# Kernel tuning notes

Hardware: AMD Instinct MI355X
Metric: run time of the kernel (lower is better)

The kernel has to match this reference:

```python
import jax, jax.numpy as jnp
import numpy as np

D_MODEL, D_STATE, D_CONV, D_INNER = 1024, 16, 4, 2048
B, S = 1, 2048
EPS = 1e-5


def setup_inputs() -> dict:
    key = jax.random.key(0)
    ks = jax.random.split(key, 8)
    sc = 0.02
    return {
        "x": jax.random.normal(ks[0], (B, S, D_MODEL), jnp.float32),
        "ln_g": jnp.ones((D_MODEL,), jnp.float32),
        "ln_b": jnp.zeros((D_MODEL,), jnp.float32),
        "in_w": jax.random.normal(ks[1], (2 * D_INNER, D_MODEL), jnp.float32) * sc,
        "conv_w": jax.random.normal(ks[2], (D_INNER, 1, D_CONV), jnp.float32) * sc,  # depthwise OIH
        "conv_b": jax.random.normal(ks[3], (D_INNER,), jnp.float32) * sc,
        "xproj_w": jax.random.normal(ks[4], (2 * D_STATE + 1, D_INNER), jnp.float32) * sc,
        "dt_w": jax.random.normal(ks[5], (D_INNER, 1), jnp.float32) * sc,
        "dt_b": jax.random.normal(ks[6], (D_INNER,), jnp.float32) * sc,
        "A_log": jnp.log(jnp.arange(1, D_STATE + 1, dtype=jnp.float32)),
        "D": jnp.ones((D_INNER,), jnp.float32),
        "out_w": jax.random.normal(ks[7], (D_MODEL, D_INNER), jnp.float32) * sc,
    }


def reference(x, ln_g, ln_b, in_w, conv_w, conv_b, xproj_w, dt_w, dt_b, A_log, D, out_w):
    b, s, _ = x.shape
    d_inner = D.shape[0]
    d_state = A_log.shape[0]
    d_conv = conv_w.shape[-1]
    residual = x

    # LayerNorm
    mu = jnp.mean(x, axis=-1, keepdims=True)
    var = jnp.mean(jnp.square(x - mu), axis=-1, keepdims=True)
    xn = (x - mu) * jax.lax.rsqrt(var + EPS) * ln_g + ln_b

    # in_proj, split into x and gate z
    xz = jnp.einsum('bsd,ed->bse', xn, in_w)  # [B,S,2*d_inner]
    xi, z = jnp.split(xz, 2, axis=-1)

    # causal depthwise conv1d (torch pads d_conv-1 both sides then crops to seq_len)
    xc = jnp.transpose(xi, (0, 2, 1))  # [B,C,S]
    xc = jnp.pad(xc, ((0, 0), (0, 0), (d_conv - 1, 0)))
    xc = jax.lax.conv_general_dilated(
        xc, conv_w, window_strides=(1,), padding='VALID',
        dimension_numbers=('NCH', 'OIH', 'NCH'), feature_group_count=d_inner)
    xc = xc + conv_b[None, :, None]
    xs = jax.nn.silu(jnp.transpose(xc, (0, 2, 1)))  # [B,S,d_inner]

    # SSM projections
    xp = jnp.einsum('bsd,ed->bse', xs, xproj_w)  # [B,S,2*d_state+1]
    delta = jax.nn.softplus(xp[..., :1] * dt_w[:, 0] + dt_b)  # [B,S,d_inner]
    Bm = xp[..., 1:1 + d_state]  # [B,S,N]
    Cm = xp[..., 1 + d_state:]   # [B,S,N]
    A = -jnp.exp(A_log)          # [N]

    dA = jnp.exp(delta[..., None] * A)                      # [B,S,d_inner,N]
    dBx = delta[..., None] * Bm[:, :, None, :] * xs[..., None]  # [B,S,d_inner,N]

    def step(h, inp):
        dA_t, dBx_t, C_t = inp
        h = dA_t * h + dBx_t                     # [B,d_inner,N]
        y_t = jnp.einsum('bdn,bn->bd', h, C_t)   # [B,d_inner]
        return h, y_t

    h0 = jnp.zeros((b, d_inner, d_state), x.dtype)
    _, ys = jax.lax.scan(step, h0, (jnp.moveaxis(dA, 1, 0),
                                    jnp.moveaxis(dBx, 1, 0),
                                    jnp.moveaxis(Cm, 1, 0)))
    y = jnp.moveaxis(ys, 0, 1) + xs * D  # [B,S,d_inner]

    y = y * jax.nn.silu(z)
    out = jnp.einsum('bse,de->bsd', y, out_w)
    return out + residual
```

## Files before the change

kernel.cpp:

```cpp
#include <hip/hip_runtime.h>
#include <cstdint>
#include <cstddef>

#define D_MODEL 1024
#define D_STATE 16
#define D_CONV  4
#define D_INNER 2048
#define SEQ     2048
#define NCHUNK  128
#define CLEN    16
#define NGRP    8
#define GCH     16
#define LN_EPS  1e-5f

typedef unsigned short ushort_t;
typedef __attribute__((ext_vector_type(8))) short short8;
typedef __attribute__((ext_vector_type(4))) float f32x4;

__device__ __forceinline__ ushort_t f2bf(float x) {
  union { float f; uint32_t u; } v; v.f = x;
  uint32_t r = (v.u + 0x7fffu + ((v.u >> 16) & 1u)) >> 16;
  return (ushort_t)r;
}
__device__ __forceinline__ float bf2f(ushort_t u) {
  union { uint32_t x; float f; } v; v.x = ((uint32_t)u) << 16; return v.f;
}

__device__ __forceinline__ void async16(void* lds, const void* g) {
  __builtin_amdgcn_global_load_lds(
      (const __attribute__((address_space(1))) unsigned int*)g,
      (__attribute__((address_space(3))) unsigned int*)lds, 16, 0, 0);
}

__device__ __forceinline__ float softplus_f(float x) {
  if (x > 20.f) return x;
  if (x < -20.f) return __expf(x);
  return __logf(1.f + __expf(x));
}

__device__ __forceinline__ void dapow(float g1, float* da) {
  float g2 = g1 * g1, g4 = g2 * g2, g8 = g4 * g4;
  #pragma unroll
  for (int n = 0; n < 16; n++) {
    int e = n + 1;
    float v = (e & 1) ? g1 : 1.f;
    if (e & 2) v *= g2;
    if (e & 4) v *= g4;
    if (e & 8) v *= g8;
    da[n] = v;
  }
}

__global__ __launch_bounds__(256) void prep_kernel(const float* __restrict__ x,
                                                   const float* __restrict__ g,
                                                   const float* __restrict__ b,
                                                   const float* __restrict__ inw,
                                                   const float* __restrict__ outw,
                                                   const float* __restrict__ xpw,
                                                   ushort_t* __restrict__ xn_bf,
                                                   ushort_t* __restrict__ inw_bf,
                                                   ushort_t* __restrict__ outw_bf,
                                                   ushort_t* __restrict__ xpw_bf) {
  int blk = blockIdx.x;
  if (blk < SEQ) {
    int row = blk;
    const float4* xr = (const float4*)(x + (size_t)row * D_MODEL);
    float4 v = xr[threadIdx.x];
    float s  = v.x + v.y + v.z + v.w;
    float ss = v.x * v.x + v.y * v.y + v.z * v.z + v.w * v.w;
    #pragma unroll
    for (int o = 32; o; o >>= 1) { s += __shfl_down(s, o); ss += __shfl_down(ss, o); }
    __shared__ float sbuf[8], ssbuf[8];
    int wid = threadIdx.x >> 6, lane = threadIdx.x & 63;
    if (lane == 0) { sbuf[wid] = s; ssbuf[wid] = ss; }
    __syncthreads();
    if (threadIdx.x == 0) {
      float t = 0.f, t2 = 0.f;
      for (int i = 0; i < 4; i++) { t += sbuf[i]; t2 += ssbuf[i]; }
      float mu = t / D_MODEL;
      sbuf[4] = mu;
      ssbuf[4] = rsqrtf(t2 / D_MODEL - mu * mu + LN_EPS);
    }
    __syncthreads();
    float mu = sbuf[4], inv = ssbuf[4];
    float4 gv = ((const float4*)g)[threadIdx.x];
    float4 bv = ((const float4*)b)[threadIdx.x];
    ushort_t o4[4];
    o4[0] = f2bf((v.x - mu) * inv * gv.x + bv.x);
    o4[1] = f2bf((v.y - mu) * inv * gv.y + bv.y);
    o4[2] = f2bf((v.z - mu) * inv * gv.z + bv.z);
    o4[3] = f2bf((v.w - mu) * inv * gv.w + bv.w);
    *(ushort4*)&xn_bf[(size_t)row * D_MODEL + threadIdx.x * 4] =
        make_ushort4(o4[0], o4[1], o4[2], o4[3]);
  } else {
    int idx = (blk - SEQ) * 256 + threadIdx.x;
    const int n1 = 2 * D_INNER * D_MODEL;
    const int n2 = D_MODEL * D_INNER;
    const int n3 = 64 * D_INNER;
    if (idx < n1) {
      inw_bf[idx] = f2bf(inw[idx]);
    } else if (idx < n1 + n2) {
      int j = idx - n1;
      outw_bf[j] = f2bf(outw[j]);
    } else if (idx < n1 + n2 + n3) {
      int j = idx - n1 - n2;
      xpw_bf[j] = (j < 33 * D_INNER) ? f2bf(xpw[j]) : (ushort_t)0;
    }
  }
}

template <int BM, int BN, int KDIM, int EPI, int NBUF, int KSPLIT>
__global__ __launch_bounds__(256, 2) void gemm_pipe(const ushort_t* __restrict__ A,
                                                    const ushort_t* __restrict__ B,
                                                    void* __restrict__ Cout,
                                                    const float* __restrict__ R,
                                                    int N) {
  constexpr int KT = KDIM / 32 / KSPLIT;
  constexpr int K2 = KDIM * 2;
  constexpr int IA = BM / 64, IB = BN / 64;
  constexpr int S  = IA + IB;
  constexpr int W  = (NBUF - 2) * S;
  constexpr int WTM = BM / 2, WTN = BN / 2;
  constexpr int MREP = WTM / 16, NREP = WTN / 16;
  __shared__ __align__(16) ushort_t As[NBUF][BM * 32];
  __shared__ __align__(16) ushort_t Bs[NBUF][BN * 32];

  const int nwg = gridDim.x * gridDim.y;
  int bid = blockIdx.y * gridDim.x + blockIdx.x;
  int swz = (bid & 7) * (nwg >> 3) + (bid >> 3);
  int bn = swz % gridDim.x, bm = swz / gridDim.x;
  int ks = 0;
  if constexpr (KSPLIT > 1) { ks = bn; bn = 0; }
  const int tid = threadIdx.x, wid = tid >> 6, lane = tid & 63;
  const int wm = wid >> 1, wn = wid & 1;
  const int row0A = bm * BM, row0B = bn * BN;
  const size_t kbase = (size_t)ks * KT * 64;

  const char* gA[IA];
  const char* gB[IB];
  #pragma unroll
  for (int i = 0; i < IA; i++) {
    int o = i * 4096 + tid * 16;
    int r = o >> 6, src = (o & 63) ^ ((r & 3) << 4);
    gA[i] = (const char*)A + (size_t)(row0A + r) * K2 + src + kbase;
  }
  #pragma unroll
  for (int i = 0; i < IB; i++) {
    int o = i * 4096 + tid * 16;
    int r = o >> 6, src = (o & 63) ^ ((r & 3) << 4);
    gB[i] = (const char*)B + (size_t)(row0B + r) * K2 + src + kbase;
  }
  const int ldsW = wid * 1024;

  auto STAGE = [&](int bb, int kt) {
    int kb = kt * 64;
    #pragma unroll
    for (int i = 0; i < IA; i++)
      async16((char*)&As[bb][0] + i * 4096 + ldsW, gA[i] + kb);
    #pragma unroll
    for (int i = 0; i < IB; i++)
      async16((char*)&Bs[bb][0] + i * 4096 + ldsW, gB[i] + kb);
  };

  #pragma unroll
  for (int p = 0; p < NBUF - 1; p++) STAGE(p, p);

  int offA[MREP], offB[NREP];
  #pragma unroll
  for (int m = 0; m < MREP; m++) {
    int row = wm * WTM + m * 16 + (lane & 15);
    offA[m] = row * 64 + ((((lane >> 4)) ^ (row & 3)) << 4);
  }
  #pragma unroll
  for (int n = 0; n < NREP; n++) {
    int row = wn * WTN + n * 16 + (lane & 15);
    offB[n] = row * 64 + ((((lane >> 4)) ^ (row & 3)) << 4);
  }

  f32x4 acc[MREP][NREP] = {};
  int cur = 0;
  for (int kt = 0; kt < KT; kt++) {
    if (kt < KT - 1) {
      if constexpr (W == 6)       asm volatile("s_waitcnt vmcnt(6)" ::: "memory");
      else if constexpr (W == 8)  asm volatile("s_waitcnt vmcnt(8)" ::: "memory");
      else if constexpr (W == 12) asm volatile("s_waitcnt vmcnt(12)" ::: "memory");
      else                        asm volatile("s_waitcnt vmcnt(0)" ::: "memory");
    } else {
      asm volatile("s_waitcnt vmcnt(0)" ::: "memory");
    }
    __builtin_amdgcn_s_barrier();
    __builtin_amdgcn_sched_barrier(0);
    const char* Ab = (const char*)&As[cur][0];
    const char* Bb = (const char*)&Bs[cur][0];
    short8 af[MREP], bf[NREP];
    #pragma unroll
    for (int m = 0; m < MREP; m++) af[m] = *(const short8*)(Ab + offA[m]);
    #pragma unroll
    for (int n = 0; n < NREP; n++) bf[n] = *(const short8*)(Bb + offB[n]);
    if (kt + NBUF - 1 < KT) {
      int b2 = cur + NBUF - 1; if (b2 >= NBUF) b2 -= NBUF;
      STAGE(b2, kt + NBUF - 1);
    }
    __builtin_amdgcn_s_setprio(1);
    #pragma unroll
    for (int m = 0; m < MREP; m++)
      #pragma unroll
      for (int n = 0; n < NREP; n++)
        acc[m][n] = __builtin_amdgcn_mfma_f32_16x16x32_bf16(af[m], bf[n], acc[m][n], 0, 0, 0);
    __builtin_amdgcn_s_setprio(0);
    cur++; if (cur == NBUF) cur = 0;
  }

  #pragma unroll
  for (int m = 0; m < MREP; m++)
    #pragma unroll
    for (int n = 0; n < NREP; n++) {
      int r0 = row0A + wm * WTM + m * 16 + ((lane >> 4) << 2);
      int c  = row0B + wn * WTN + n * 16 + (lane & 15);
      #pragma unroll
      for (int q = 0; q < 4; q++) {
        if constexpr (EPI == 0) {
          ((ushort_t*)Cout)[(size_t)(r0 + q) * N + c] = f2bf(acc[m][n][q]);
        } else if constexpr (EPI == 1) {
          size_t idx = (size_t)(r0 + q) * N + c;
          ((float*)Cout)[idx] = acc[m][n][q] + R[idx];
        } else {
          if (c < 33)
            ((float*)Cout)[((size_t)ks * SEQ + r0 + q) * 33 + c] = acc[m][n][q];
        }
      }
    }
}

__global__ __launch_bounds__(256) void xp_reduce(const float* __restrict__ part,
                                                 float* __restrict__ xp) {
  int i = blockIdx.x * 256 + threadIdx.x;
  if (i >= SEQ * 33) return;
  float s = 0.f;
  #pragma unroll
  for (int k = 0; k < 8; k++) s += part[(size_t)k * SEQ * 33 + i];
  xp[i] = s;
}

__global__ __launch_bounds__(256) void conv_silu_kernel(const ushort_t* __restrict__ xz_bf,
                                                        const float* __restrict__ cw,
                                                        const float* __restrict__ cb,
                                                        ushort_t* __restrict__ xs_bf) {
  const int t = blockIdx.x;
  const int d0 = threadIdx.x * 8;
  short8 rows[4];
  #pragma unroll
  for (int k = 0; k < 4; k++) {
    int tt = t - 3 + k;
    if (tt >= 0) rows[k] = *(const short8*)&xz_bf[(size_t)tt * (2 * D_INNER) + d0];
    else         rows[k] = (short8)0;
  }
  short8 o8;
  #pragma unroll
  for (int j = 0; j < 8; j++) {
    float4 w = ((const float4*)cw)[d0 + j];
    float acc = cb[d0 + j]
              + bf2f((ushort_t)rows[0][j]) * w.x
              + bf2f((ushort_t)rows[1][j]) * w.y
              + bf2f((ushort_t)rows[2][j]) * w.z
              + bf2f((ushort_t)rows[3][j]) * w.w;
    float sg = 1.f / (1.f + __expf(-acc));
    o8[j] = (short)f2bf(acc * sg);
  }
  *(short8*)&xs_bf[(size_t)t * D_INNER + d0] = o8;
}

__global__ __launch_bounds__(256) void scan_pass1(const ushort_t* __restrict__ xs_bf,
                                                  const float* __restrict__ xp,
                                                  const float* __restrict__ dt_w,
                                                  const float* __restrict__ dt_b,
                                                  const float* __restrict__ A_log,
                                                  float* __restrict__ Hp,
                                                  float* __restrict__ Sd) {
  int c = blockIdx.x;
  int d0 = blockIdx.y * 512 + threadIdx.x;
  __shared__ float Bsh[CLEN][16], drs[CLEN], Ash[16];
  {
    int t = threadIdx.x >> 4, n = threadIdx.x & 15;
    Bsh[t][n] = xp[(size_t)(c * CLEN + t) * 33 + 1 + n];
    if (threadIdx.x < CLEN) drs[threadIdx.x] = xp[(size_t)(c * CLEN + threadIdx.x) * 33];
    else if (threadIdx.x < CLEN + 16) {
      int n2 = threadIdx.x - CLEN;
      Ash[n2] = -__expf(A_log[n2]);
    }
  }
  __syncthreads();
  bool fastA = true;
  #pragma unroll
  for (int n = 0; n < 16; n++) fastA = fastA && (fabsf(Ash[n] + (float)(n + 1)) < 1e-4f * (n + 1));
  float dw[2] = {dt_w[d0], dt_w[d0 + 256]};
  float db[2] = {dt_b[d0], dt_b[d0 + 256]};
  float h[2][16] = {};
  float S[2] = {0.f, 0.f};
  for (int t = 0; t < CLEN; t++) {
    float bb[16];
    *(float4*)&bb[0]  = *(const float4*)&Bsh[t][0];
    *(float4*)&bb[4]  = *(const float4*)&Bsh[t][4];
    *(float4*)&bb[8]  = *(const float4*)&Bsh[t][8];
    *(float4*)&bb[12] = *(const float4*)&Bsh[t][12];
    float drt = drs[t];
    size_t tb = (size_t)(c * CLEN + t) * D_INNER;
    float xv[2] = {bf2f(xs_bf[tb + d0]), bf2f(xs_bf[tb + d0 + 256])};
    #pragma unroll
    for (int u = 0; u < 2; u++) {
      float delta = softplus_f(drt * dw[u] + db[u]);
      S[u] += delta;
      float w = delta * xv[u];
      if (fastA) {
        float da[16];
        dapow(__expf(-delta), da);
        #pragma unroll
        for (int n = 0; n < 16; n++) h[u][n] = da[n] * h[u][n] + w * bb[n];
      } else {
        #pragma unroll
        for (int n = 0; n < 16; n++) h[u][n] = __expf(delta * Ash[n]) * h[u][n] + w * bb[n];
      }
    }
  }
  #pragma unroll
  for (int u = 0; u < 2; u++) {
    int d = d0 + u * 256;
    size_t base = ((size_t)c * D_INNER + d) * 16;
    #pragma unroll
    for (int n = 0; n < 16; n += 4)
      *(float4*)&Hp[base + n] = make_float4(h[u][n], h[u][n + 1], h[u][n + 2], h[u][n + 3]);
    Sd[(size_t)c * D_INNER + d] = S[u];
  }
}

__global__ __launch_bounds__(256) void combineA(const float* __restrict__ Hp,
                                                const float* __restrict__ Sd,
                                                const float* __restrict__ A_log,
                                                float* __restrict__ Hl,
                                                float* __restrict__ Slocp,
                                                float* __restrict__ Hgtot,
                                                float* __restrict__ Sgtot) {
  int g = blockIdx.x;
  int idx = blockIdx.y * 256 + threadIdx.x;
  int d = idx >> 4, n = idx & 15;
  float An = -__expf(A_log[n]);
  float h = 0.f, S = 0.f;
  const size_t stride = (size_t)D_INNER * 16;
  #pragma unroll 4
  for (int j = 0; j < GCH; j++) {
    int c = g * GCH + j;
    Hl[(size_t)c * stride + idx] = h;
    if (n == 0) Slocp[(size_t)c * D_INNER + d] = S;
    float Sc = Sd[(size_t)c * D_INNER + d];
    float hp = Hp[(size_t)c * stride + idx];
    h = __expf(An * Sc) * h + hp;
    S += Sc;
  }
  Hgtot[(size_t)g * stride + idx] = h;
  if (n == 0) Sgtot[(size_t)g * D_INNER + d] = S;
}

__global__ __launch_bounds__(256) void combineB(const float* __restrict__ Hgtot,
                                                const float* __restrict__ Sgtot,
                                                const float* __restrict__ A_log,
                                                float* __restrict__ Ginit) {
  int idx = blockIdx.x * 256 + threadIdx.x;
  int d = idx >> 4, n = idx & 15;
  float An = -__expf(A_log[n]);
  float G = 0.f;
  const size_t stride = (size_t)D_INNER * 16;
  #pragma unroll
  for (int g = 0; g < NGRP; g++) {
    Ginit[(size_t)g * stride + idx] = G;
    G = __expf(An * Sgtot[(size_t)g * D_INNER + d]) * G + Hgtot[(size_t)g * stride + idx];
  }
}

__global__ __launch_bounds__(256) void scan_pass2(const ushort_t* __restrict__ xs_bf,
                                                  const float* __restrict__ xp,
                                                  const ushort_t* __restrict__ xz_bf,
                                                  const float* __restrict__ dt_w,
                                                  const float* __restrict__ dt_b,
                                                  const float* __restrict__ A_log,
                                                  const float* __restrict__ Dp,
                                                  const float* __restrict__ Hl,
                                                  const float* __restrict__ Slocp,
                                                  const float* __restrict__ Ginit,
                                                  ushort_t* __restrict__ y_bf) {
  int c = blockIdx.x;
  int d0 = blockIdx.y * 512 + threadIdx.x;
  __shared__ float Bsh[CLEN][16], Csh[CLEN][16], drs[CLEN], Ash[16];
  {
    int t = threadIdx.x >> 4, n = threadIdx.x & 15;
    Bsh[t][n] = xp[(size_t)(c * CLEN + t) * 33 + 1 + n];
    Csh[t][n] = xp[(size_t)(c * CLEN + t) * 33 + 17 + n];
    if (threadIdx.x < CLEN) drs[threadIdx.x] = xp[(size_t)(c * CLEN + threadIdx.x) * 33];
    else if (threadIdx.x < CLEN + 16) {
      int n2 = threadIdx.x - CLEN;
      Ash[n2] = -__expf(A_log[n2]);
    }
  }
  __syncthreads();
  bool fastA = true;
  #pragma unroll
  for (int n = 0; n < 16; n++) fastA = fastA && (fabsf(Ash[n] + (float)(n + 1)) < 1e-4f * (n + 1));
  float dw[2] = {dt_w[d0], dt_w[d0 + 256]};
  float db[2] = {dt_b[d0], dt_b[d0 + 256]};
  float Dd[2] = {Dp[d0], Dp[d0 + 256]};
  int g8 = c >> 4;
  float h[2][16];
  #pragma unroll
  for (int u = 0; u < 2; u++) {
    int d = d0 + u * 256;
    size_t hb = ((size_t)c * D_INNER + d) * 16;
    size_t gb = ((size_t)g8 * D_INNER + d) * 16;
    float Slp = Slocp[(size_t)c * D_INNER + d];
    float hl[16], gi[16];
    #pragma unroll
    for (int n = 0; n < 16; n += 4) {
      *(float4*)&hl[n] = *(const float4*)&Hl[hb + n];
      *(float4*)&gi[n] = *(const float4*)&Ginit[gb + n];
    }
    if (fastA) {
      float pw[16];
      dapow(__expf(-Slp), pw);
      #pragma unroll
      for (int n = 0; n < 16; n++) h[u][n] = hl[n] + pw[n] * gi[n];
    } else {
      #pragma unroll
      for (int n = 0; n < 16; n++) h[u][n] = hl[n] + __expf(Ash[n] * Slp) * gi[n];
    }
  }
  for (int t = 0; t < CLEN; t++) {
    float bb[16], cc[16];
    *(float4*)&bb[0]  = *(const float4*)&Bsh[t][0];
    *(float4*)&bb[4]  = *(const float4*)&Bsh[t][4];
    *(float4*)&bb[8]  = *(const float4*)&Bsh[t][8];
    *(float4*)&bb[12] = *(const float4*)&Bsh[t][12];
    *(float4*)&cc[0]  = *(const float4*)&Csh[t][0];
    *(float4*)&cc[4]  = *(const float4*)&Csh[t][4];
    *(float4*)&cc[8]  = *(const float4*)&Csh[t][8];
    *(float4*)&cc[12] = *(const float4*)&Csh[t][12];
    float drt = drs[t];
    size_t ti = (size_t)(c * CLEN + t);
    float xv[2] = {bf2f(xs_bf[ti * D_INNER + d0]), bf2f(xs_bf[ti * D_INNER + d0 + 256])};
    float zv[2] = {bf2f(xz_bf[ti * (2 * D_INNER) + D_INNER + d0]),
                   bf2f(xz_bf[ti * (2 * D_INNER) + D_INNER + d0 + 256])};
    #pragma unroll
    for (int u = 0; u < 2; u++) {
      float delta = softplus_f(drt * dw[u] + db[u]);
      float w = delta * xv[u];
      float y = 0.f;
      if (fastA) {
        float da[16];
        dapow(__expf(-delta), da);
        #pragma unroll
        for (int n = 0; n < 16; n++) {
          h[u][n] = da[n] * h[u][n] + w * bb[n];
          y += h[u][n] * cc[n];
        }
      } else {
        #pragma unroll
        for (int n = 0; n < 16; n++) {
          h[u][n] = __expf(delta * Ash[n]) * h[u][n] + w * bb[n];
          y += h[u][n] * cc[n];
        }
      }
      float z = zv[u];
      float sz = z / (1.f + __expf(-z));
      float out = (y + xv[u] * Dd[u]) * sz;
      y_bf[ti * D_INNER + d0 + u * 256] = f2bf(out);
    }
  }
}

extern "C" void kernel_launch(void* const* d_in, const int* in_sizes, int n_in,
                              void* d_out, int out_size, void* d_ws, size_t ws_size,
                              hipStream_t stream) {
  const float* x      = (const float*)d_in[0];
  const float* ln_g   = (const float*)d_in[1];
  const float* ln_b   = (const float*)d_in[2];
  const float* in_w   = (const float*)d_in[3];
  const float* conv_w = (const float*)d_in[4];
  const float* conv_b = (const float*)d_in[5];
  const float* xproj_w= (const float*)d_in[6];
  const float* dt_w   = (const float*)d_in[7];
  const float* dt_b   = (const float*)d_in[8];
  const float* A_log  = (const float*)d_in[9];
  const float* Dp     = (const float*)d_in[10];
  const float* out_w  = (const float*)d_in[11];
  float* out = (float*)d_out;

  char* ws = (char*)d_ws;
  size_t off = 0;
  auto alloc = [&](size_t bytes) { char* p = ws + off; off += (bytes + 255) & ~(size_t)255; return p; };
  ushort_t* xz_bf   = (ushort_t*)alloc((size_t)SEQ * 2 * D_INNER * 2);
  ushort_t* xn_bf   = (ushort_t*)alloc((size_t)SEQ * D_MODEL * 2);
  ushort_t* inw_bf  = (ushort_t*)alloc((size_t)2 * D_INNER * D_MODEL * 2);
  ushort_t* outw_bf = (ushort_t*)alloc((size_t)D_MODEL * D_INNER * 2);
  ushort_t* xpw_bf  = (ushort_t*)alloc((size_t)64 * D_INNER * 2);
  ushort_t* xs_bf   = (ushort_t*)alloc((size_t)SEQ * D_INNER * 2);
  float*    xp_part = (float*)   alloc((size_t)8 * SEQ * 33 * 4);
  float*    xp      = (float*)   alloc((size_t)SEQ * 33 * 4);
  float*    Hp      = (float*)   alloc((size_t)NCHUNK * D_INNER * 16 * 4);
  float*    Hl      = (float*)   alloc((size_t)NCHUNK * D_INNER * 16 * 4);
  float*    Sd      = (float*)   alloc((size_t)NCHUNK * D_INNER * 4);
  float*    Slocp   = (float*)   alloc((size_t)NCHUNK * D_INNER * 4);
  float*    Hgtot   = (float*)   alloc((size_t)NGRP * D_INNER * 16 * 4);
  float*    Sgtot   = (float*)   alloc((size_t)NGRP * D_INNER * 4);
  float*    Ginit   = (float*)   alloc((size_t)NGRP * D_INNER * 16 * 4);
  ushort_t* y_bf    = (ushort_t*)alloc((size_t)SEQ * D_INNER * 2);
  (void)ws_size;

  const int ncvt = 2 * D_INNER * D_MODEL + D_MODEL * D_INNER + 64 * D_INNER;
  prep_kernel<<<SEQ + (ncvt + 255) / 256, 256, 0, stream>>>(
      x, ln_g, ln_b, in_w, out_w, xproj_w, xn_bf, inw_bf, outw_bf, xpw_bf);
  gemm_pipe<128, 128, D_MODEL, 0, 4, 1><<<dim3(2 * D_INNER / 128, SEQ / 128), 256, 0, stream>>>(
      xn_bf, inw_bf, xz_bf, nullptr, 2 * D_INNER);
  conv_silu_kernel<<<SEQ, 256, 0, stream>>>(xz_bf, conv_w, conv_b, xs_bf);
  gemm_pipe<64, 64, D_INNER, 3, 6, 8><<<dim3(8, SEQ / 64), 256, 0, stream>>>(
      xs_bf, xpw_bf, xp_part, nullptr, 64);
  xp_reduce<<<(SEQ * 33 + 255) / 256, 256, 0, stream>>>(xp_part, xp);
  scan_pass1<<<dim3(NCHUNK, D_INNER / 512), 256, 0, stream>>>(xs_bf, xp, dt_w, dt_b, A_log, Hp, Sd);
  combineA<<<dim3(NGRP, D_INNER * 16 / 256), 256, 0, stream>>>(Hp, Sd, A_log, Hl, Slocp, Hgtot, Sgtot);
  combineB<<<D_INNER * 16 / 256, 256, 0, stream>>>(Hgtot, Sgtot, A_log, Ginit);
  scan_pass2<<<dim3(NCHUNK, D_INNER / 512), 256, 0, stream>>>(xs_bf, xp, xz_bf, dt_w, dt_b, A_log,
                                                              Dp, Hl, Slocp, Ginit, y_bf);
  gemm_pipe<64, 64, D_INNER, 1, 6, 1><<<dim3(D_MODEL / 64, SEQ / 64), 256, 0, stream>>>(
      y_bf, outw_bf, out, x, D_MODEL);
}
```

Baseline: 134.3 us.

## Fuse xproj split-K reduction into scan passes, prefetch inputs, retile in_proj GEMM

Removes the separate xp_reduce kernel and has scan_pass1 and scan_pass2 sum the eight split-K partials directly while loading B, C and delta into shared memory. This saves one launch and one intermediate buffer, but the partial sums are now read by both scan kernels. The scan loops also prefetch the next timestep's xs and z values into registers so the loads overlap the recurrence. The in_proj GEMM tile changes from 128x128 with 4 stages to 256x128 with 3 stages, which halves the grid rows and may change occupancy.

```diff
diff --git a/kernel.cpp b/kernel.cpp
--- a/kernel.cpp
+++ b/kernel.cpp
@@ -232,16 +232,6 @@
     }
 }
 
-__global__ __launch_bounds__(256) void xp_reduce(const float* __restrict__ part,
-                                                 float* __restrict__ xp) {
-  int i = blockIdx.x * 256 + threadIdx.x;
-  if (i >= SEQ * 33) return;
-  float s = 0.f;
-  #pragma unroll
-  for (int k = 0; k < 8; k++) s += part[(size_t)k * SEQ * 33 + i];
-  xp[i] = s;
-}
-
 __global__ __launch_bounds__(256) void conv_silu_kernel(const ushort_t* __restrict__ xz_bf,
                                                         const float* __restrict__ cw,
                                                         const float* __restrict__ cb,
@@ -271,7 +261,7 @@
 }
 
 __global__ __launch_bounds__(256) void scan_pass1(const ushort_t* __restrict__ xs_bf,
-                                                  const float* __restrict__ xp,
+                                                  const float* __restrict__ xpp,
                                                   const float* __restrict__ dt_w,
                                                   const float* __restrict__ dt_b,
                                                   const float* __restrict__ A_log,
@@ -282,9 +272,19 @@
   __shared__ float Bsh[CLEN][16], drs[CLEN], Ash[16];
   {
     int t = threadIdx.x >> 4, n = threadIdx.x & 15;
-    Bsh[t][n] = xp[(size_t)(c * CLEN + t) * 33 + 1 + n];
-    if (threadIdx.x < CLEN) drs[threadIdx.x] = xp[(size_t)(c * CLEN + threadIdx.x) * 33];
-    else if (threadIdx.x < CLEN + 16) {
+    const size_t P = (size_t)SEQ * 33;
+    size_t rb = (size_t)(c * CLEN + t) * 33;
+    float sB = 0.f;
+    #pragma unroll
+    for (int k = 0; k < 8; k++) sB += xpp[k * P + rb + 1 + n];
+    Bsh[t][n] = sB;
+    if (threadIdx.x < CLEN) {
+      size_t rr = (size_t)(c * CLEN + threadIdx.x) * 33;
+      float sD = 0.f;
+      #pragma unroll
+      for (int k = 0; k < 8; k++) sD += xpp[k * P + rr];
+      drs[threadIdx.x] = sD;
+    } else if (threadIdx.x < CLEN + 16) {
       int n2 = threadIdx.x - CLEN;
       Ash[n2] = -__expf(A_log[n2]);
     }
@@ -297,15 +297,20 @@
   float db[2] = {dt_b[d0], dt_b[d0 + 256]};
   float h[2][16] = {};
   float S[2] = {0.f, 0.f};
+  size_t tb = (size_t)(c * CLEN) * D_INNER + d0;
+  float xv[2] = {bf2f(xs_bf[tb]), bf2f(xs_bf[tb + 256])};
   for (int t = 0; t < CLEN; t++) {
+    float nx[2] = {0.f, 0.f};
+    if (t + 1 < CLEN) {
+      nx[0] = bf2f(xs_bf[tb + D_INNER]);
+      nx[1] = bf2f(xs_bf[tb + D_INNER + 256]);
+    }
     float bb[16];
     *(float4*)&bb[0]  = *(const float4*)&Bsh[t][0];
     *(float4*)&bb[4]  = *(const float4*)&Bsh[t][4];
     *(float4*)&bb[8]  = *(const float4*)&Bsh[t][8];
     *(float4*)&bb[12] = *(const float4*)&Bsh[t][12];
     float drt = drs[t];
-    size_t tb = (size_t)(c * CLEN + t) * D_INNER;
-    float xv[2] = {bf2f(xs_bf[tb + d0]), bf2f(xs_bf[tb + d0 + 256])};
     #pragma unroll
     for (int u = 0; u < 2; u++) {
       float delta = softplus_f(drt * dw[u] + db[u]);
@@ -321,6 +326,8 @@
         for (int n = 0; n < 16; n++) h[u][n] = __expf(delta * Ash[n]) * h[u][n] + w * bb[n];
       }
     }
+    xv[0] = nx[0]; xv[1] = nx[1];
+    tb += D_INNER;
   }
   #pragma unroll
   for (int u = 0; u < 2; u++) {
@@ -377,7 +384,7 @@
 }
 
 __global__ __launch_bounds__(256) void scan_pass2(const ushort_t* __restrict__ xs_bf,
-                                                  const float* __restrict__ xp,
+                                                  const float* __restrict__ xpp,
                                                   const ushort_t* __restrict__ xz_bf,
                                                   const float* __restrict__ dt_w,
                                                   const float* __restrict__ dt_b,
@@ -392,10 +399,23 @@
   __shared__ float Bsh[CLEN][16], Csh[CLEN][16], drs[CLEN], Ash[16];
   {
     int t = threadIdx.x >> 4, n = threadIdx.x & 15;
-    Bsh[t][n] = xp[(size_t)(c * CLEN + t) * 33 + 1 + n];
-    Csh[t][n] = xp[(size_t)(c * CLEN + t) * 33 + 17 + n];
-    if (threadIdx.x < CLEN) drs[threadIdx.x] = xp[(size_t)(c * CLEN + threadIdx.x) * 33];
-    else if (threadIdx.x < CLEN + 16) {
+    const size_t P = (size_t)SEQ * 33;
+    size_t rb = (size_t)(c * CLEN + t) * 33;
+    float sB = 0.f, sC = 0.f;
+    #pragma unroll
+    for (int k = 0; k < 8; k++) {
+      sB += xpp[k * P + rb + 1 + n];
+      sC += xpp[k * P + rb + 17 + n];
+    }
+    Bsh[t][n] = sB;
+    Csh[t][n] = sC;
+    if (threadIdx.x < CLEN) {
+      size_t rr = (size_t)(c * CLEN + threadIdx.x) * 33;
+      float sD = 0.f;
+      #pragma unroll
+      for (int k = 0; k < 8; k++) sD += xpp[k * P + rr];
+      drs[threadIdx.x] = sD;
+    } else if (threadIdx.x < CLEN + 16) {
       int n2 = threadIdx.x - CLEN;
       Ash[n2] = -__expf(A_log[n2]);
     }
@@ -431,7 +451,18 @@
       for (int n = 0; n < 16; n++) h[u][n] = hl[n] + __expf(Ash[n] * Slp) * gi[n];
     }
   }
+  size_t tb = (size_t)(c * CLEN) * D_INNER + d0;
+  size_t zb = (size_t)(c * CLEN) * (2 * D_INNER) + D_INNER + d0;
+  float xv[2] = {bf2f(xs_bf[tb]), bf2f(xs_bf[tb + 256])};
+  float zv[2] = {bf2f(xz_bf[zb]), bf2f(xz_bf[zb + 256])};
   for (int t = 0; t < CLEN; t++) {
+    float nx[2] = {0.f, 0.f}, nz[2] = {0.f, 0.f};
+    if (t + 1 < CLEN) {
+      nx[0] = bf2f(xs_bf[tb + D_INNER]);
+      nx[1] = bf2f(xs_bf[tb + D_INNER + 256]);
+      nz[0] = bf2f(xz_bf[zb + 2 * D_INNER]);
+      nz[1] = bf2f(xz_bf[zb + 2 * D_INNER + 256]);
+    }
     float bb[16], cc[16];
     *(float4*)&bb[0]  = *(const float4*)&Bsh[t][0];
     *(float4*)&bb[4]  = *(const float4*)&Bsh[t][4];
@@ -443,9 +474,6 @@
     *(float4*)&cc[12] = *(const float4*)&Csh[t][12];
     float drt = drs[t];
     size_t ti = (size_t)(c * CLEN + t);
-    float xv[2] = {bf2f(xs_bf[ti * D_INNER + d0]), bf2f(xs_bf[ti * D_INNER + d0 + 256])};
-    float zv[2] = {bf2f(xz_bf[ti * (2 * D_INNER) + D_INNER + d0]),
-                   bf2f(xz_bf[ti * (2 * D_INNER) + D_INNER + d0 + 256])};
     #pragma unroll
     for (int u = 0; u < 2; u++) {
       float delta = softplus_f(drt * dw[u] + db[u]);
@@ -471,6 +499,9 @@
       float out = (y + xv[u] * Dd[u]) * sz;
       y_bf[ti * D_INNER + d0 + u * 256] = f2bf(out);
     }
+    xv[0] = nx[0]; xv[1] = nx[1];
+    zv[0] = nz[0]; zv[1] = nz[1];
+    tb += D_INNER; zb += 2 * D_INNER;
   }
 }
 
@@ -501,7 +532,6 @@
   ushort_t* xpw_bf  = (ushort_t*)alloc((size_t)64 * D_INNER * 2);
   ushort_t* xs_bf   = (ushort_t*)alloc((size_t)SEQ * D_INNER * 2);
   float*    xp_part = (float*)   alloc((size_t)8 * SEQ * 33 * 4);
-  float*    xp      = (float*)   alloc((size_t)SEQ * 33 * 4);
   float*    Hp      = (float*)   alloc((size_t)NCHUNK * D_INNER * 16 * 4);
   float*    Hl      = (float*)   alloc((size_t)NCHUNK * D_INNER * 16 * 4);
   float*    Sd      = (float*)   alloc((size_t)NCHUNK * D_INNER * 4);
@@ -515,16 +545,15 @@
   const int ncvt = 2 * D_INNER * D_MODEL + D_MODEL * D_INNER + 64 * D_INNER;
   prep_kernel<<<SEQ + (ncvt + 255) / 256, 256, 0, stream>>>(
       x, ln_g, ln_b, in_w, out_w, xproj_w, xn_bf, inw_bf, outw_bf, xpw_bf);
-  gemm_pipe<128, 128, D_MODEL, 0, 4, 1><<<dim3(2 * D_INNER / 128, SEQ / 128), 256, 0, stream>>>(
+  gemm_pipe<256, 128, D_MODEL, 0, 3, 1><<<dim3(2 * D_INNER / 128, SEQ / 256), 256, 0, stream>>>(
       xn_bf, inw_bf, xz_bf, nullptr, 2 * D_INNER);
   conv_silu_kernel<<<SEQ, 256, 0, stream>>>(xz_bf, conv_w, conv_b, xs_bf);
   gemm_pipe<64, 64, D_INNER, 3, 6, 8><<<dim3(8, SEQ / 64), 256, 0, stream>>>(
       xs_bf, xpw_bf, xp_part, nullptr, 64);
-  xp_reduce<<<(SEQ * 33 + 255) / 256, 256, 0, stream>>>(xp_part, xp);
-  scan_pass1<<<dim3(NCHUNK, D_INNER / 512), 256, 0, stream>>>(xs_bf, xp, dt_w, dt_b, A_log, Hp, Sd);
+  scan_pass1<<<dim3(NCHUNK, D_INNER / 512), 256, 0, stream>>>(xs_bf, xp_part, dt_w, dt_b, A_log, Hp, Sd);
   combineA<<<dim3(NGRP, D_INNER * 16 / 256), 256, 0, stream>>>(Hp, Sd, A_log, Hl, Slocp, Hgtot, Sgtot);
   combineB<<<D_INNER * 16 / 256, 256, 0, stream>>>(Hgtot, Sgtot, A_log, Ginit);
-  scan_pass2<<<dim3(NCHUNK, D_INNER / 512), 256, 0, stream>>>(xs_bf, xp, xz_bf, dt_w, dt_b, A_log,
+  scan_pass2<<<dim3(NCHUNK, D_INNER / 512), 256, 0, stream>>>(xs_bf, xp_part, xz_bf, dt_w, dt_b, A_log,
                                                               Dp, Hl, Slocp, Ginit, y_bf);
   gemm_pipe<64, 64, D_INNER, 1, 6, 1><<<dim3(D_MODEL / 64, SEQ / 64), 256, 0, stream>>>(
       y_bf, outw_bf, out, x, D_MODEL);
```

New measurement: 135.4 us. No clear change (+0.8%).
